# Kernel tuning notes

Measured on AMD Instinct MI355X. Metric: run time of the kernel, lower is better.

Reference implementation:

```python
import jax, jax.numpy as jnp
import numpy as np

S = 2        # number of scales (init default)
ALPHA = 1.0  # loss weight (init default)


def _local_pod_ss(D, n_scales):
    """Sum of squares of (P_n - P_o) over all scales/windows.

    D = h_n - h_o, shape [B, C, W, H]. Because POD is linear in x,
    POD(h_n window) - POD(h_o window) == POD(D window), and the final
    torch.norm(P_n - P_o, 2) is the Frobenius norm over the full concat,
    so we accumulate squared window-POD values of D and sqrt at the end.
    Window sums are computed once via prefix sums (integral along one axis)
    instead of the original O(W^2 H^2) re-summation loop.
    """
    B, C, W, H = D.shape
    ss = jnp.zeros((), D.dtype)
    d = 1
    for s in range(n_scales):
        w, h = W // d, H // d
        if w == 0 or h == 0:
            break
        nI, nJ = W - w, H - h  # number of window start positions (torch range(0, W-w))
        if nI > 0 and nJ > 0:
            # 'left' term: sum over rows (dim=2) of each window, divided by w
            cs2 = jnp.pad(jnp.cumsum(D, axis=2), ((0, 0), (0, 0), (1, 0), (0, 0)))
            row = cs2[:, :, w:w + nI, :] - cs2[:, :, :nI, :]              # [B,C,nI,H]
            jidx = jnp.arange(nJ)[:, None] + jnp.arange(h)[None, :]       # [nJ,h]
            left = row[:, :, :, jidx] / w                                 # [B,C,nI,nJ,h]
            ss = ss + jnp.sum(left * left)
            # 'right' term: sum over cols (dim=3) of each window, divided by h
            cs3 = jnp.pad(jnp.cumsum(D, axis=3), ((0, 0), (0, 0), (0, 0), (1, 0)))
            col = cs3[:, :, :, h:h + nJ] - cs3[:, :, :, :nJ]              # [B,C,W,nJ]
            iidx = jnp.arange(nI)[:, None] + jnp.arange(w)[None, :]       # [nI,w]
            right = col[:, :, iidx, :] / h                                # [B,C,nI,w,nJ]
            ss = ss + jnp.sum(right * right)
        d *= 2
    return ss


def setup_inputs() -> dict:
    key = jax.random.key(0)
    k1, k2 = jax.random.split(key)
    new_f = jax.random.normal(k1, (16, 512, 32, 32), dtype=jnp.float32)
    old_f = jax.random.normal(k2, (16, 512, 32, 32), dtype=jnp.float32)
    return {"new_f": new_f, "old_f": old_f}


def reference(new_f, old_f):
    # forward loops over dict keys; here new_f/old_f model a single-key dict,
    # so loss = 1e-6 + local_pod(h_n, h_o) and divisor is len(new_f)+1 == 2.
    D = new_f - old_f
    loss = jnp.asarray(1e-6, new_f.dtype) + jnp.sqrt(_local_pod_ss(D, S))
    return ALPHA * loss / 2.0
```

## Files before the change

kernel.cpp:

```cpp
#include <hip/hip_runtime.h>
#include <math.h>


#define TILE_PAD 33
#define TILE_STRIDE (32 * TILE_PAD)
#define NTILES 4
#define BLOCK_FLOATS (NTILES * 1024)
#define NBLOCKS 2048

__global__ __launch_bounds__(256) void pod_partial(const float* __restrict__ nf,
                                                   const float* __restrict__ of,
                                                   float* __restrict__ partial) {
    __shared__ float ds[NTILES * TILE_STRIDE];
    const int tid = threadIdx.x;
    const size_t base = (size_t)blockIdx.x * BLOCK_FLOATS;
    const float4* nf4 = reinterpret_cast<const float4*>(nf + base);
    const float4* of4 = reinterpret_cast<const float4*>(of + base);

    float4 a[NTILES], b[NTILES];
#pragma unroll
    for (int it = 0; it < NTILES; ++it) a[it] = nf4[it * 256 + tid];
#pragma unroll
    for (int it = 0; it < NTILES; ++it) b[it] = of4[it * 256 + tid];

#pragma unroll
    for (int it = 0; it < NTILES; ++it) {
        int e = (it * 256 + tid) * 4;
        int tile = e >> 10, r = (e >> 5) & 31, c = e & 31;
        float* dst = &ds[tile * TILE_STRIDE + r * TILE_PAD + c];
        dst[0] = a[it].x - b[it].x;
        dst[1] = a[it].y - b[it].y;
        dst[2] = a[it].z - b[it].z;
        dst[3] = a[it].w - b[it].w;
    }
    __syncthreads();

    const int item = tid & 127;
    const int tile = item >> 5;
    const int lane = item & 31;
    float v[32];
    if (tid < 128) {
        const float* p = &ds[tile * TILE_STRIDE + lane];
#pragma unroll
        for (int k = 0; k < 32; ++k) v[k] = p[k * TILE_PAD];
    } else {
        const float* p = &ds[tile * TILE_STRIDE + lane * TILE_PAD];
#pragma unroll
        for (int k = 0; k < 32; ++k) v[k] = p[k];
    }
    float W = 0.0f;
#pragma unroll
    for (int k = 0; k < 16; ++k) W += v[k];
    float s2 = W * W;
#pragma unroll
    for (int i = 1; i < 16; ++i) { W += v[i + 15] - v[i - 1]; s2 += W * W; }
    float wgt = (lane < 16) ? (float)(lane + 1) : (float)(31 - lane);
    float acc = wgt * s2 * (1.0f / 256.0f);

#pragma unroll
    for (int off = 32; off > 0; off >>= 1) acc += __shfl_down(acc, off, 64);
    __shared__ float wsum[4];
    if ((tid & 63) == 0) wsum[tid >> 6] = acc;
    __syncthreads();
    if (tid == 0) partial[blockIdx.x] = (wsum[0] + wsum[1]) + (wsum[2] + wsum[3]);
}

__global__ __launch_bounds__(256) void pod_final(const float* __restrict__ partial,
                                                 float* __restrict__ out) {
    __shared__ float sh[256];
    int tid = threadIdx.x;
    float a = 0.0f;
#pragma unroll
    for (int i = 0; i < NBLOCKS / 256; ++i) a += partial[i * 256 + tid];
    sh[tid] = a;
    __syncthreads();
    for (int s = 128; s > 0; s >>= 1) {
        if (tid < s) sh[tid] += sh[tid + s];
        __syncthreads();
    }
    if (tid == 0) out[0] = 0.5f * (1e-6f + sqrtf(sh[0]));
}

extern "C" void kernel_launch(void* const* d_in, const int* in_sizes, int n_in,
                              void* d_out, int out_size, void* d_ws, size_t ws_size,
                              hipStream_t stream) {
    const float* nf = (const float*)d_in[0];
    const float* of = (const float*)d_in[1];
    float* out = (float*)d_out;
    float* partial = (float*)d_ws;

    hipLaunchKernelGGL(pod_partial, dim3(NBLOCKS), dim3(256), 0, stream, nf, of, partial);
    hipLaunchKernelGGL(pod_final, dim3(1), dim3(256), 0, stream, partial, out);
}
```

Before: 17.53 us.

## Fuse final reduction via fixed-point 64-bit atomics with last-block detection

```diff
diff --git a/kernel.cpp b/kernel.cpp
--- a/kernel.cpp
+++ b/kernel.cpp
@@ -7,12 +7,22 @@
 #define NTILES 4
 #define BLOCK_FLOATS (NTILES * 1024)
 #define NBLOCKS 2048
+#define NGROUPS 32
+#define GROUP_LAST 63ull
+#define ACC_STRIDE 8
+#define FP_SCALE 4096.0f
 
-__global__ __launch_bounds__(256) void pod_partial(const float* __restrict__ nf,
-                                                   const float* __restrict__ of,
-                                                   float* __restrict__ partial) {
+__global__ __launch_bounds__(256) void pod_fused(const float* __restrict__ nf,
+                                                 const float* __restrict__ of,
+                                                 unsigned long long* __restrict__ acc64,
+                                                 unsigned* __restrict__ lvl2,
+                                                 float* __restrict__ out) {
     __shared__ float ds[NTILES * TILE_STRIDE];
+    __shared__ float wsum[4];
+    __shared__ int sh_last;
     const int tid = threadIdx.x;
+    if (tid == 0) sh_last = 0;
+
     const size_t base = (size_t)blockIdx.x * BLOCK_FLOATS;
     const float4* nf4 = reinterpret_cast<const float4*>(nf + base);
     const float4* of4 = reinterpret_cast<const float4*>(of + base);
@@ -59,26 +69,36 @@
 
 #pragma unroll
     for (int off = 32; off > 0; off >>= 1) acc += __shfl_down(acc, off, 64);
-    __shared__ float wsum[4];
     if ((tid & 63) == 0) wsum[tid >> 6] = acc;
     __syncthreads();
-    if (tid == 0) partial[blockIdx.x] = (wsum[0] + wsum[1]) + (wsum[2] + wsum[3]);
-}
 
-__global__ __launch_bounds__(256) void pod_final(const float* __restrict__ partial,
-                                                 float* __restrict__ out) {
-    __shared__ float sh[256];
-    int tid = threadIdx.x;
-    float a = 0.0f;
+    if (tid == 0) {
+        float total = (wsum[0] + wsum[1]) + (wsum[2] + wsum[3]);
+        unsigned long long q = (unsigned long long)(total * FP_SCALE);
+        const int grp = blockIdx.x & (NGROUPS - 1);
+        unsigned long long old = atomicAdd(&acc64[grp * ACC_STRIDE], (q << 12) | 1ull);
+        if ((old & 0xFFFull) == GROUP_LAST) {
+            unsigned inc = 1u;
+            asm volatile("" : "+v"(inc) : "v"((unsigned)old));
+            unsigned l2 = atomicAdd(lvl2, inc);
+            if (l2 == NGROUPS - 1u) sh_last = 1;
+        }
+    }
+    __syncthreads();
+
+    if (sh_last && tid < 64) {
+        long long myv = 0;
+        if (tid < NGROUPS) {
+            unsigned long long vraw = atomicAdd(&acc64[tid * ACC_STRIDE], 0ull);
+            myv = (long long)((vraw - (GROUP_LAST + 1ull)) >> 12);
+        }
 #pragma unroll
-    for (int i = 0; i < NBLOCKS / 256; ++i) a += partial[i * 256 + tid];
-    sh[tid] = a;
-    __syncthreads();
-    for (int s = 128; s > 0; s >>= 1) {
-        if (tid < s) sh[tid] += sh[tid + s];
-        __syncthreads();
+        for (int off = 32; off > 0; off >>= 1) myv += __shfl_down(myv, off, 64);
+        if (tid == 0) {
+            double ss = (double)myv * (1.0 / (double)FP_SCALE);
+            out[0] = 0.5f * (1e-6f + sqrtf((float)ss));
+        }
     }
-    if (tid == 0) out[0] = 0.5f * (1e-6f + sqrtf(sh[0]));
 }
 
 extern "C" void kernel_launch(void* const* d_in, const int* in_sizes, int n_in,
@@ -87,8 +107,11 @@
     const float* nf = (const float*)d_in[0];
     const float* of = (const float*)d_in[1];
     float* out = (float*)d_out;
-    float* partial = (float*)d_ws;
 
-    hipLaunchKernelGGL(pod_partial, dim3(NBLOCKS), dim3(256), 0, stream, nf, of, partial);
-    hipLaunchKernelGGL(pod_final, dim3(1), dim3(256), 0, stream, partial, out);
+    unsigned long long* acc64 = (unsigned long long*)d_ws;
+    unsigned* lvl2 = (unsigned*)((char*)d_ws + NGROUPS * ACC_STRIDE * 8);
+
+    hipMemsetAsync(d_ws, 0, 4096, stream);
+    hipLaunchKernelGGL(pod_fused, dim3(NBLOCKS), dim3(256), 0, stream,
+                       nf, of, acc64, lvl2, out);
 }
```

New measurement: 22.72 us. 1.3x slower.
